# Kernel tuning notes

Hardware: AMD Instinct MI355X
Metric: run time of the kernel (lower is better)

Reference implementation:

```python
import math
import jax, jax.numpy as jnp
import numpy as np

H = 16  # num_heads

def get_alibi_slopes(n):
    def pow2_slopes(n):
        start = 2 ** (-2 ** (-(math.log2(n) - 3)))
        return [start * start ** i for i in range(n)]
    if math.log2(n).is_integer():
        return pow2_slopes(n)
    c = 2 ** math.floor(math.log2(n))
    return pow2_slopes(c) + get_alibi_slopes(2 * c)[0::2][: n - c]

def alibi_bias(num_heads, L, dtype=jnp.float32):
    slopes = jnp.asarray(get_alibi_slopes(num_heads), dtype=dtype)  # [H]
    pos = jnp.arange(L)
    rel = (pos[None, :] - pos[:, None]).astype(dtype)               # [L, L] = x - y
    bias = slopes[:, None, None] * rel[None, :, :]                  # [H, L, L]
    causal = pos[None, :] <= pos[:, None]                           # tril mask
    return jnp.where(causal[None, :, :], bias, -jnp.inf)


def setup_inputs() -> dict:
    key = jax.random.key(0)
    ks = jax.random.split(key, 4)
    D = 1024
    B, L = 2, 2048
    s_in = 1.0 / math.sqrt(D)
    return {
        "x": jax.random.normal(ks[0], (B, L, D), dtype=jnp.float32),
        "w_in": jax.random.normal(ks[1], (D, 3 * D), dtype=jnp.float32) * s_in,
        "b_in": jnp.zeros((3 * D,), dtype=jnp.float32),
        "w_out": jax.random.normal(ks[2], (D, D), dtype=jnp.float32) * s_in,
        "b_out": jnp.zeros((D,), dtype=jnp.float32),
    }


def reference(x, w_in, b_in, w_out, b_out):
    B, L, D = x.shape
    dh = D // H
    qkv = x @ w_in + b_in                                   # [B, L, 3D]
    q, k, v = jnp.split(qkv, 3, axis=-1)
    # [B, L, D] -> [B, H, L, dh]
    def heads(t):
        return t.reshape(B, L, H, dh).transpose(0, 2, 1, 3)
    q, k, v = heads(q), heads(k), heads(v)
    scores = jnp.einsum("bhqd,bhkd->bhqk", q, k) / math.sqrt(dh)
    scores = scores + alibi_bias(H, L, scores.dtype)[None]  # [B, H, L, L]
    attn = jax.nn.softmax(scores, axis=-1)
    out = jnp.einsum("bhqk,bhkd->bhqd", attn, v)            # [B, H, L, dh]
    out = out.transpose(0, 2, 1, 3).reshape(B, L, D)
    return out @ w_out + b_out
```

## Files before the change

### kernel.cpp

```cpp
#include <hip/hip_runtime.h>
#include <stdint.h>
#include <math.h>

#define NH 16
#define DH 64
#define SEQ 2048
#define DMODEL 1024

typedef short short8 __attribute__((ext_vector_type(8)));
typedef short short4v __attribute__((ext_vector_type(4)));
typedef float f32x4 __attribute__((ext_vector_type(4)));
typedef __bf16 bf16x4 __attribute__((ext_vector_type(4)));

__device__ __forceinline__ short f2bf(float f) {
  __bf16 h = (__bf16)f;
  return __builtin_bit_cast(short, h);
}
__device__ __forceinline__ short4v cvt4(f32x4 v) {
  bf16x4 b = __builtin_convertvector(v, bf16x4);
  return __builtin_bit_cast(short4v, b);
}
__device__ __forceinline__ float fast_exp2(float x) {
#if __has_builtin(__builtin_amdgcn_exp2f)
  return __builtin_amdgcn_exp2f(x);
#else
  return exp2f(x);
#endif
}

typedef const __attribute__((address_space(1))) uint32_t* gp_t;
typedef __attribute__((address_space(3))) uint32_t* lp_t;
__device__ __forceinline__ void async16(const short* g, short* l) {
  __builtin_amdgcn_global_load_lds((gp_t)g, (lp_t)l, 16, 0, 0);
}

__device__ __forceinline__ void transpose_tile(const float* __restrict__ in,
                                               short* __restrict__ out, int R, int C,
                                               int t, int tilesX, int tid) {
  __shared__ float tile[32][33];
  const int tx = tid & 31, ty = tid >> 5;
  const int c0 = (t % tilesX) * 32, r0 = (t / tilesX) * 32;
#pragma unroll
  for (int i = 0; i < 4; ++i)
    tile[ty + i * 8][tx] = in[(size_t)(r0 + ty + i * 8) * C + c0 + tx];
  __syncthreads();
#pragma unroll
  for (int i = 0; i < 4; ++i)
    out[(size_t)(c0 + ty + i * 8) * R + r0 + tx] = f2bf(tile[tx][ty + i * 8]);
}

__global__ void k_prep(const float* __restrict__ x, short* __restrict__ xb,
                       const float* __restrict__ w_in, short* __restrict__ w_in_t,
                       const float* __restrict__ w_out, short* __restrict__ w_out_t) {
  const int tid = threadIdx.x;
  const int blk = blockIdx.x;
  if (blk < 4096) {
    const int i = blk * 256 + tid;
    f32x4 v = ((const f32x4*)x)[i];
    ((short4v*)xb)[i] = cvt4(v);
  } else if (blk < 4096 + 3072) {
    transpose_tile(w_in, w_in_t, 1024, 3072, blk - 4096, 96, tid);
  } else {
    transpose_tile(w_out, w_out_t, 1024, 1024, blk - 7168, 32, tid);
  }
}

template <int MODE>
__launch_bounds__(256, 3)
__global__ void k_gemm(const short* __restrict__ A, const short* __restrict__ Bt,
                       const float* __restrict__ bias, float* __restrict__ Cf,
                       short* __restrict__ qo, short* __restrict__ ko,
                       short* __restrict__ vo) {
  constexpr int KD = 1024;
  __shared__ __align__(16) short As[128 * 64];
  __shared__ __align__(16) short Bs[128 * 64];
  const int tid = threadIdx.x;
  const int wave = tid >> 6, lane = tid & 63;
  const int quad = lane >> 4, l16 = lane & 15;
  const int wm = wave >> 1, wn = wave & 1;
  const int tM = blockIdx.y * 128, tN = blockIdx.x * 128;

  const short* pA[4];
  const short* pB[4];
  short* lA[4];
  short* lB[4];
#pragma unroll
  for (int t = 0; t < 4; ++t) {
    const int c = t * 256 + tid;
    const int row = c >> 3, gch = (c & 7) ^ (row & 7);
    pA[t] = A + (size_t)(tM + row) * KD + gch * 8;
    pB[t] = Bt + (size_t)(tN + row) * KD + gch * 8;
    lA[t] = &As[c * 8];
    lB[t] = &Bs[c * 8];
  }

  const int sw = l16 & 7;
  const int col0 = (quad ^ sw) << 3;
  const int col1 = col0 ^ 32;

  f32x4 acc[4][4] = {};

  for (int k0 = 0; k0 < KD; k0 += 64) {
    __syncthreads();
#pragma unroll
    for (int t = 0; t < 4; ++t) {
      async16(pA[t] + k0, lA[t]);
      async16(pB[t] + k0, lB[t]);
    }
    __syncthreads();
#pragma unroll
    for (int kh = 0; kh < 2; ++kh) {
      const int col = kh ? col1 : col0;
      short8 af[4], bfr[4];
#pragma unroll
      for (int i = 0; i < 4; ++i)
        af[i] = *(const short8*)&As[(wm * 64 + i * 16 + l16) * 64 + col];
#pragma unroll
      for (int i = 0; i < 4; ++i)
        bfr[i] = *(const short8*)&Bs[(wn * 64 + i * 16 + l16) * 64 + col];
#pragma unroll
      for (int i = 0; i < 4; ++i)
#pragma unroll
        for (int j = 0; j < 4; ++j)
          acc[i][j] = __builtin_amdgcn_mfma_f32_16x16x32_bf16(af[i], bfr[j], acc[i][j], 0, 0, 0);
    }
  }

  const int rbase = tM + wm * 64 + quad * 4;
#pragma unroll
  for (int i = 0; i < 4; ++i) {
#pragma unroll
    for (int j = 0; j < 4; ++j) {
      const int col = tN + wn * 64 + j * 16 + l16;
      const float bi = bias[col];
      if (MODE == 0) {
        const int which = col >> 10;
        const int h = (col & 1023) >> 6, d = col & 63;
        if (which == 2) {
          const int row0 = rbase + i * 16;
          const int b = row0 >> 11, li0 = row0 & 2047;
          f32x4 t;
#pragma unroll
          for (int rr = 0; rr < 4; ++rr) t[rr] = acc[i][j][rr] + bi;
          *(short4v*)&vo[(((size_t)(b * NH + h)) * DH + d) * SEQ + li0] = cvt4(t);
        } else {
          short* dst = (which == 0) ? qo : ko;
#pragma unroll
          for (int rr = 0; rr < 4; ++rr) {
            const int row = rbase + i * 16 + rr;
            const int b = row >> 11, li = row & 2047;
            dst[(((size_t)(b * NH + h)) * SEQ + li) * DH + d] = f2bf(acc[i][j][rr] + bi);
          }
        }
      } else {
#pragma unroll
        for (int rr = 0; rr < 4; ++rr) {
          const int row = rbase + i * 16 + rr;
          Cf[(size_t)row * DMODEL + col] = acc[i][j][rr] + bi;
        }
      }
    }
  }
}

__launch_bounds__(256)
__global__ void k_attn(const short* __restrict__ q, const short* __restrict__ k,
                       const short* __restrict__ vt, short* __restrict__ o) {
  __shared__ __align__(16) short Qs[64 * 64];
  __shared__ __align__(16) short Ks[64 * 64];
  __shared__ __align__(16) short Vs[64 * 64];
  __shared__ __align__(16) short Ps[4][16 * 64];
  const int tid = threadIdx.x;
  const int wave = tid >> 6, lane = tid & 63;
  const int quad = lane >> 4, l16 = lane & 15;
  const int sw = l16 & 7;
  const int qt = 31 - (blockIdx.x >> 5);
  const int bh = blockIdx.x & 31;
  const int h = bh & (NH - 1);
  const size_t base = (size_t)bh * SEQ * DH;
  const float LOG2E = 1.44269504088896f;
  const float slope2 = exp2f(-0.5f * (float)(h + 1)) * LOG2E;
  const float scale2 = 0.125f * LOG2E;
  const float FM = 12.0f;

  const int c0i = tid, c1i = 256 + tid;
  const int r0 = c0i >> 3, ch0 = (c0i & 7) ^ (r0 & 7);
  const int r1 = c1i >> 3, ch1 = (c1i & 7) ^ (r1 & 7);
  const int qk_off0 = r0 * DH + ch0 * 8;
  const int qk_off1 = r1 * DH + ch1 * 8;
  const int v_off0 = r0 * SEQ + ch0 * 8;
  const int v_off1 = r1 * SEQ + ch1 * 8;
  short* lQ0 = &Qs[c0i * 8]; short* lQ1 = &Qs[c1i * 8];
  short* lK0 = &Ks[c0i * 8]; short* lK1 = &Ks[c1i * 8];
  short* lV0 = &Vs[c0i * 8]; short* lV1 = &Vs[c1i * 8];

  const int col0 = ((quad ^ sw) << 3);
  const int col1 = col0 ^ 32;
  int psoff[4];
#pragma unroll
  for (int in = 0; in < 4; ++in)
    psoff[in] = l16 * 64 + (((2 * in + (quad >> 1)) ^ sw) << 3) + (quad & 1) * 4;
  const int qlim4 = wave * 16 + l16 - 4 * quad;
  const float s64 = slope2 * 64.0f;
  float rc[4];
#pragma unroll
  for (int r = 0; r < 4; ++r) rc[r] = slope2 * (float)r;

  const int q0 = qt * 64;
  {
    const short* qb = q + base + (size_t)q0 * DH;
    async16(qb + qk_off0, lQ0);
    async16(qb + qk_off1, lQ1);
  }
  __syncthreads();
  const short8 qb0 = *(const short8*)&Qs[(wave * 16 + l16) * 64 + col0];
  const short8 qb1 = *(const short8*)&Qs[(wave * 16 + l16) * 64 + col1];

  f32x4 accO[4] = {};
  float lsum = 0.f;
  const int qrow = q0 + wave * 16 + l16;
  const float qoff = -slope2 * (float)qrow - FM + slope2 * (float)(4 * quad);
  float inoff[4];
#pragma unroll
  for (int in = 0; in < 4; ++in)
    inoff[in] = qoff + slope2 * (float)(16 * in);

  const short* kp = k + base;
  const short* vp = vt + base;
  for (int kt = 0; kt <= qt; ++kt) {
    __syncthreads();
    async16(kp + qk_off0, lK0);
    async16(kp + qk_off1, lK1);
    async16(vp + v_off0, lV0);
    async16(vp + v_off1, lV1);
    kp += 64 * DH;
    vp += 64;
    __syncthreads();

    f32x4 s[4];
#pragma unroll
    for (int in = 0; in < 4; ++in) {
      const short8 ka0 = *(const short8*)&Ks[(in * 16 + l16) * 64 + col0];
      const short8 ka1 = *(const short8*)&Ks[(in * 16 + l16) * 64 + col1];
      f32x4 t = {};
      t = __builtin_amdgcn_mfma_f32_16x16x32_bf16(ka0, qb0, t, 0, 0, 0);
      t = __builtin_amdgcn_mfma_f32_16x16x32_bf16(ka1, qb1, t, 0, 0, 0);
      s[in] = t;
    }

    if (kt == qt) {
#pragma unroll
      for (int in = 0; in < 4; ++in) {
        f32x4 p;
#pragma unroll
        for (int r = 0; r < 4; ++r) {
          float val = fast_exp2(fmaf(s[in][r], scale2, inoff[in] + rc[r]));
          val = (16 * in + r <= qlim4) ? val : 0.f;
          p[r] = val;
          lsum += val;
        }
        *(short4v*)&Ps[wave][psoff[in]] = cvt4(p);
      }
    } else {
#pragma unroll
      for (int in = 0; in < 4; ++in) {
        f32x4 p;
#pragma unroll
        for (int r = 0; r < 4; ++r) {
          float val = fast_exp2(fmaf(s[in][r], scale2, inoff[in] + rc[r]));
          p[r] = val;
          lsum += val;
        }
        *(short4v*)&Ps[wave][psoff[in]] = cvt4(p);
      }
    }
#pragma unroll
    for (int in = 0; in < 4; ++in) inoff[in] += s64;

    const short8 pa0 = *(const short8*)&Ps[wave][l16 * 64 + col0];
    const short8 pa1 = *(const short8*)&Ps[wave][l16 * 64 + col1];
#pragma unroll
    for (int i = 0; i < 4; ++i) {
      const short8 va0 = *(const short8*)&Vs[(i * 16 + l16) * 64 + col0];
      const short8 va1 = *(const short8*)&Vs[(i * 16 + l16) * 64 + col1];
      accO[i] = __builtin_amdgcn_mfma_f32_16x16x32_bf16(va0, pa0, accO[i], 0, 0, 0);
      accO[i] = __builtin_amdgcn_mfma_f32_16x16x32_bf16(va1, pa1, accO[i], 0, 0, 0);
    }
  }

  lsum += __shfl_xor(lsum, 16, 64);
  lsum += __shfl_xor(lsum, 32, 64);
  const float inv = 1.0f / lsum;

  const int b = bh >> 4;
  short* ob = o + ((((size_t)b * SEQ + qrow) * NH + h) * DH + 4 * quad);
#pragma unroll
  for (int i = 0; i < 4; ++i) {
    f32x4 t;
#pragma unroll
    for (int r = 0; r < 4; ++r) t[r] = accO[i][r] * inv;
    *(short4v*)&ob[16 * i] = cvt4(t);
  }
}

extern "C" void kernel_launch(void* const* d_in, const int* in_sizes, int n_in,
                              void* d_out, int out_size, void* d_ws, size_t ws_size,
                              hipStream_t stream) {
  const float* x = (const float*)d_in[0];
  const float* w_in = (const float*)d_in[1];
  const float* b_in = (const float*)d_in[2];
  const float* w_out = (const float*)d_in[3];
  const float* b_out = (const float*)d_in[4];
  float* out = (float*)d_out;

  char* ws = (char*)d_ws;
  short* xb = (short*)(ws);
  short* w_in_t = (short*)(ws + (8u << 20));
  short* w_out_t = (short*)(ws + (14u << 20));
  short* qv = (short*)(ws + (16u << 20));
  short* kv = (short*)(ws + (24u << 20));
  short* vv = (short*)(ws + (32u << 20));
  short* ao = (short*)(ws + (40u << 20));

  k_prep<<<8192, 256, 0, stream>>>(x, xb, w_in, w_in_t, w_out, w_out_t);
  k_gemm<0><<<dim3(24, 32), 256, 0, stream>>>(xb, w_in_t, b_in, nullptr, qv, kv, vv);
  k_attn<<<1024, 256, 0, stream>>>(qv, kv, vv, ao);
  k_gemm<1><<<dim3(8, 32), 256, 0, stream>>>(ao, w_out_t, b_out, out, nullptr, nullptr, nullptr);
}
```

Measured before the change: 173.8 us.

## Load K/V fragments directly to registers, prefetch K, compute row sums via MFMA

The attention kernel drops the shared-memory staging of Q, K and V tiles and the two block-wide barriers per iteration. Each wave now loads its MFMA operand fragments straight from global memory into registers, and K for the next tile is prefetched by double-buffering registers. The softmax denominator is computed with an extra MFMA against a vector of ones instead of per-lane sums plus shuffles. The cost is redundant global loads across the four waves, since each wave loads the full K/V tile that was previously shared, plus higher register pressure. The row sum is also now taken from the bf16-rounded probabilities.

```diff
diff --git a/kernel.cpp b/kernel.cpp
--- a/kernel.cpp
+++ b/kernel.cpp
@@ -166,9 +166,6 @@
 __launch_bounds__(256)
 __global__ void k_attn(const short* __restrict__ q, const short* __restrict__ k,
                        const short* __restrict__ vt, short* __restrict__ o) {
-  __shared__ __align__(16) short Qs[64 * 64];
-  __shared__ __align__(16) short Ks[64 * 64];
-  __shared__ __align__(16) short Vs[64 * 64];
   __shared__ __align__(16) short Ps[4][16 * 64];
   const int tid = threadIdx.x;
   const int wave = tid >> 6, lane = tid & 63;
@@ -183,70 +180,67 @@
   const float scale2 = 0.125f * LOG2E;
   const float FM = 12.0f;
 
-  const int c0i = tid, c1i = 256 + tid;
-  const int r0 = c0i >> 3, ch0 = (c0i & 7) ^ (r0 & 7);
-  const int r1 = c1i >> 3, ch1 = (c1i & 7) ^ (r1 & 7);
-  const int qk_off0 = r0 * DH + ch0 * 8;
-  const int qk_off1 = r1 * DH + ch1 * 8;
-  const int v_off0 = r0 * SEQ + ch0 * 8;
-  const int v_off1 = r1 * SEQ + ch1 * 8;
-  short* lQ0 = &Qs[c0i * 8]; short* lQ1 = &Qs[c1i * 8];
-  short* lK0 = &Ks[c0i * 8]; short* lK1 = &Ks[c1i * 8];
-  short* lV0 = &Vs[c0i * 8]; short* lV1 = &Vs[c1i * 8];
-
-  const int col0 = ((quad ^ sw) << 3);
+  const int col0 = (quad ^ sw) << 3;
   const int col1 = col0 ^ 32;
   int psoff[4];
 #pragma unroll
   for (int in = 0; in < 4; ++in)
     psoff[in] = l16 * 64 + (((2 * in + (quad >> 1)) ^ sw) << 3) + (quad & 1) * 4;
   const int qlim4 = wave * 16 + l16 - 4 * quad;
+
+  const int q0 = qt * 64;
+  const int qrow = q0 + wave * 16 + l16;
+  const short* qp = q + base + (size_t)qrow * DH + quad * 8;
+  const short8 qb0 = *(const short8*)qp;
+  const short8 qb1 = *(const short8*)(qp + 32);
+
+  short8 ones;
+#pragma unroll
+  for (int j = 0; j < 8; ++j) ones[j] = (short)0x3F80;
+
+  f32x4 accO[4] = {};
+  f32x4 accL = {};
+  const float qoff = -slope2 * (float)qrow - FM + slope2 * (float)(4 * quad);
+  float inoff[4];
+#pragma unroll
+  for (int in = 0; in < 4; ++in)
+    inoff[in] = qoff + slope2 * (float)(16 * in);
   const float s64 = slope2 * 64.0f;
   float rc[4];
 #pragma unroll
   for (int r = 0; r < 4; ++r) rc[r] = slope2 * (float)r;
 
-  const int q0 = qt * 64;
-  {
-    const short* qb = q + base + (size_t)q0 * DH;
-    async16(qb + qk_off0, lQ0);
-    async16(qb + qk_off1, lQ1);
-  }
-  __syncthreads();
-  const short8 qb0 = *(const short8*)&Qs[(wave * 16 + l16) * 64 + col0];
-  const short8 qb1 = *(const short8*)&Qs[(wave * 16 + l16) * 64 + col1];
-
-  f32x4 accO[4] = {};
-  float lsum = 0.f;
-  const int qrow = q0 + wave * 16 + l16;
-  const float qoff = -slope2 * (float)qrow - FM + slope2 * (float)(4 * quad);
-  float inoff[4];
-#pragma unroll
-  for (int in = 0; in < 4; ++in)
-    inoff[in] = qoff + slope2 * (float)(16 * in);
-
-  const short* kp = k + base;
-  const short* vp = vt + base;
-  for (int kt = 0; kt <= qt; ++kt) {
-    __syncthreads();
-    async16(kp + qk_off0, lK0);
-    async16(kp + qk_off1, lK1);
-    async16(vp + v_off0, lV0);
-    async16(vp + v_off1, lV1);
-    kp += 64 * DH;
-    vp += 64;
-    __syncthreads();
-
+  const short* kfb = k + base + (size_t)l16 * DH + quad * 8;
+  const short* vfb = vt + base + (size_t)l16 * SEQ + quad * 8;
+
+  auto loadK = [&](int kt, short8* kr) {
+    const short* p = kfb + (size_t)(kt * 64) * DH;
+#pragma unroll
+    for (int in = 0; in < 4; ++in) {
+      kr[2 * in] = *(const short8*)(p + (size_t)(in * 16) * DH);
+      kr[2 * in + 1] = *(const short8*)(p + (size_t)(in * 16) * DH + 32);
+    }
+  };
+
+  auto step = [&](int kt, const short8* kr, short8* kn, bool pf) {
     f32x4 s[4];
 #pragma unroll
     for (int in = 0; in < 4; ++in) {
-      const short8 ka0 = *(const short8*)&Ks[(in * 16 + l16) * 64 + col0];
-      const short8 ka1 = *(const short8*)&Ks[(in * 16 + l16) * 64 + col1];
       f32x4 t = {};
-      t = __builtin_amdgcn_mfma_f32_16x16x32_bf16(ka0, qb0, t, 0, 0, 0);
-      t = __builtin_amdgcn_mfma_f32_16x16x32_bf16(ka1, qb1, t, 0, 0, 0);
+      t = __builtin_amdgcn_mfma_f32_16x16x32_bf16(kr[2 * in], qb0, t, 0, 0, 0);
+      t = __builtin_amdgcn_mfma_f32_16x16x32_bf16(kr[2 * in + 1], qb1, t, 0, 0, 0);
       s[in] = t;
     }
+    short8 vr[8];
+    {
+      const short* p = vfb + kt * 64;
+#pragma unroll
+      for (int i = 0; i < 4; ++i) {
+        vr[2 * i] = *(const short8*)(p + (size_t)(i * 16) * SEQ);
+        vr[2 * i + 1] = *(const short8*)(p + (size_t)(i * 16) * SEQ + 32);
+      }
+    }
+    if (pf) loadK(kt + 1, kn);
 
     if (kt == qt) {
 #pragma unroll
@@ -255,9 +249,7 @@
 #pragma unroll
         for (int r = 0; r < 4; ++r) {
           float val = fast_exp2(fmaf(s[in][r], scale2, inoff[in] + rc[r]));
-          val = (16 * in + r <= qlim4) ? val : 0.f;
-          p[r] = val;
-          lsum += val;
+          p[r] = (16 * in + r <= qlim4) ? val : 0.f;
         }
         *(short4v*)&Ps[wave][psoff[in]] = cvt4(p);
       }
@@ -266,11 +258,8 @@
       for (int in = 0; in < 4; ++in) {
         f32x4 p;
 #pragma unroll
-        for (int r = 0; r < 4; ++r) {
-          float val = fast_exp2(fmaf(s[in][r], scale2, inoff[in] + rc[r]));
-          p[r] = val;
-          lsum += val;
-        }
+        for (int r = 0; r < 4; ++r)
+          p[r] = fast_exp2(fmaf(s[in][r], scale2, inoff[in] + rc[r]));
         *(short4v*)&Ps[wave][psoff[in]] = cvt4(p);
       }
     }
@@ -279,19 +268,26 @@
 
     const short8 pa0 = *(const short8*)&Ps[wave][l16 * 64 + col0];
     const short8 pa1 = *(const short8*)&Ps[wave][l16 * 64 + col1];
+    accL = __builtin_amdgcn_mfma_f32_16x16x32_bf16(ones, pa0, accL, 0, 0, 0);
+    accL = __builtin_amdgcn_mfma_f32_16x16x32_bf16(ones, pa1, accL, 0, 0, 0);
 #pragma unroll
     for (int i = 0; i < 4; ++i) {
-      const short8 va0 = *(const short8*)&Vs[(i * 16 + l16) * 64 + col0];
-      const short8 va1 = *(const short8*)&Vs[(i * 16 + l16) * 64 + col1];
-      accO[i] = __builtin_amdgcn_mfma_f32_16x16x32_bf16(va0, pa0, accO[i], 0, 0, 0);
-      accO[i] = __builtin_amdgcn_mfma_f32_16x16x32_bf16(va1, pa1, accO[i], 0, 0, 0);
-    }
-  }
-
-  lsum += __shfl_xor(lsum, 16, 64);
-  lsum += __shfl_xor(lsum, 32, 64);
-  const float inv = 1.0f / lsum;
-
+      accO[i] = __builtin_amdgcn_mfma_f32_16x16x32_bf16(vr[2 * i], pa0, accO[i], 0, 0, 0);
+      accO[i] = __builtin_amdgcn_mfma_f32_16x16x32_bf16(vr[2 * i + 1], pa1, accO[i], 0, 0, 0);
+    }
+  };
+
+  short8 kA[8], kB[8];
+  loadK(0, kA);
+  int kt = 0;
+  for (;;) {
+    step(kt, kA, kB, kt < qt);
+    if (++kt > qt) break;
+    step(kt, kB, kA, kt < qt);
+    if (++kt > qt) break;
+  }
+
+  const float inv = 1.0f / accL[0];
   const int b = bh >> 4;
   short* ob = o + ((((size_t)b * SEQ + qrow) * NH + h) * DH + 4 * quad);
 #pragma unroll
```

After: 250.2 us. 43.9% more time.

## Double-buffer K/V tiles in attention, load Q from global, MFMA row sums

Applied to the files above, without the earlier changes.

Double-buffers the K and V shared-memory tiles so the async load of the next key block overlaps compute on the current one, using one barrier per iteration instead of two. Q fragments are loaded straight from global memory into registers, dropping the Q shared tile and its barrier. The softmax denominator now comes from an MFMA against a vector of bf16 ones instead of per-lane scalar adds and cross-lane shuffles. This doubles K/V LDS use and sums bf16-rounded probabilities, which matches what the PV product sees but changes rounding.

```diff
diff --git a/kernel.cpp b/kernel.cpp
--- a/kernel.cpp
+++ b/kernel.cpp
@@ -166,9 +166,8 @@
 __launch_bounds__(256)
 __global__ void k_attn(const short* __restrict__ q, const short* __restrict__ k,
                        const short* __restrict__ vt, short* __restrict__ o) {
-  __shared__ __align__(16) short Qs[64 * 64];
-  __shared__ __align__(16) short Ks[64 * 64];
-  __shared__ __align__(16) short Vs[64 * 64];
+  __shared__ __align__(16) short Ks[2][64 * 64];
+  __shared__ __align__(16) short Vs[2][64 * 64];
   __shared__ __align__(16) short Ps[4][16 * 64];
   const int tid = threadIdx.x;
   const int wave = tid >> 6, lane = tid & 63;
@@ -190,9 +189,6 @@
   const int qk_off1 = r1 * DH + ch1 * 8;
   const int v_off0 = r0 * SEQ + ch0 * 8;
   const int v_off1 = r1 * SEQ + ch1 * 8;
-  short* lQ0 = &Qs[c0i * 8]; short* lQ1 = &Qs[c1i * 8];
-  short* lK0 = &Ks[c0i * 8]; short* lK1 = &Ks[c1i * 8];
-  short* lV0 = &Vs[c0i * 8]; short* lV1 = &Vs[c1i * 8];
 
   const int col0 = ((quad ^ sw) << 3);
   const int col1 = col0 ^ 32;
@@ -201,47 +197,56 @@
   for (int in = 0; in < 4; ++in)
     psoff[in] = l16 * 64 + (((2 * in + (quad >> 1)) ^ sw) << 3) + (quad & 1) * 4;
   const int qlim4 = wave * 16 + l16 - 4 * quad;
+
+  const int q0 = qt * 64;
+  const int qrow = q0 + wave * 16 + l16;
+  const short* qp = q + base + (size_t)qrow * DH + quad * 8;
+  const short8 qb0 = *(const short8*)qp;
+  const short8 qb1 = *(const short8*)(qp + 32);
+
+  short8 ones;
+#pragma unroll
+  for (int j = 0; j < 8; ++j) ones[j] = (short)0x3F80;
+
+  f32x4 accO[4] = {};
+  f32x4 accL = {};
+  const float qoff = -slope2 * (float)qrow - FM + slope2 * (float)(4 * quad);
+  float inoff[4];
+#pragma unroll
+  for (int in = 0; in < 4; ++in)
+    inoff[in] = qoff + slope2 * (float)(16 * in);
   const float s64 = slope2 * 64.0f;
   float rc[4];
 #pragma unroll
   for (int r = 0; r < 4; ++r) rc[r] = slope2 * (float)r;
 
-  const int q0 = qt * 64;
-  {
-    const short* qb = q + base + (size_t)q0 * DH;
-    async16(qb + qk_off0, lQ0);
-    async16(qb + qk_off1, lQ1);
-  }
-  __syncthreads();
-  const short8 qb0 = *(const short8*)&Qs[(wave * 16 + l16) * 64 + col0];
-  const short8 qb1 = *(const short8*)&Qs[(wave * 16 + l16) * 64 + col1];
-
-  f32x4 accO[4] = {};
-  float lsum = 0.f;
-  const int qrow = q0 + wave * 16 + l16;
-  const float qoff = -slope2 * (float)qrow - FM + slope2 * (float)(4 * quad);
-  float inoff[4];
-#pragma unroll
-  for (int in = 0; in < 4; ++in)
-    inoff[in] = qoff + slope2 * (float)(16 * in);
-
   const short* kp = k + base;
   const short* vp = vt + base;
+
+  async16(kp + qk_off0, &Ks[0][c0i * 8]);
+  async16(kp + qk_off1, &Ks[0][c1i * 8]);
+  async16(vp + v_off0, &Vs[0][c0i * 8]);
+  async16(vp + v_off1, &Vs[0][c1i * 8]);
+  kp += 64 * DH;
+  vp += 64;
+  __syncthreads();
+
   for (int kt = 0; kt <= qt; ++kt) {
-    __syncthreads();
-    async16(kp + qk_off0, lK0);
-    async16(kp + qk_off1, lK1);
-    async16(vp + v_off0, lV0);
-    async16(vp + v_off1, lV1);
-    kp += 64 * DH;
-    vp += 64;
-    __syncthreads();
+    const int cur = kt & 1, nxt = cur ^ 1;
+    if (kt < qt) {
+      async16(kp + qk_off0, &Ks[nxt][c0i * 8]);
+      async16(kp + qk_off1, &Ks[nxt][c1i * 8]);
+      async16(vp + v_off0, &Vs[nxt][c0i * 8]);
+      async16(vp + v_off1, &Vs[nxt][c1i * 8]);
+      kp += 64 * DH;
+      vp += 64;
+    }
 
     f32x4 s[4];
 #pragma unroll
     for (int in = 0; in < 4; ++in) {
-      const short8 ka0 = *(const short8*)&Ks[(in * 16 + l16) * 64 + col0];
-      const short8 ka1 = *(const short8*)&Ks[(in * 16 + l16) * 64 + col1];
+      const short8 ka0 = *(const short8*)&Ks[cur][(in * 16 + l16) * 64 + col0];
+      const short8 ka1 = *(const short8*)&Ks[cur][(in * 16 + l16) * 64 + col1];
       f32x4 t = {};
       t = __builtin_amdgcn_mfma_f32_16x16x32_bf16(ka0, qb0, t, 0, 0, 0);
       t = __builtin_amdgcn_mfma_f32_16x16x32_bf16(ka1, qb1, t, 0, 0, 0);
@@ -255,9 +260,7 @@
 #pragma unroll
         for (int r = 0; r < 4; ++r) {
           float val = fast_exp2(fmaf(s[in][r], scale2, inoff[in] + rc[r]));
-          val = (16 * in + r <= qlim4) ? val : 0.f;
-          p[r] = val;
-          lsum += val;
+          p[r] = (16 * in + r <= qlim4) ? val : 0.f;
         }
         *(short4v*)&Ps[wave][psoff[in]] = cvt4(p);
       }
@@ -266,11 +269,8 @@
       for (int in = 0; in < 4; ++in) {
         f32x4 p;
 #pragma unroll
-        for (int r = 0; r < 4; ++r) {
-          float val = fast_exp2(fmaf(s[in][r], scale2, inoff[in] + rc[r]));
-          p[r] = val;
-          lsum += val;
-        }
+        for (int r = 0; r < 4; ++r)
+          p[r] = fast_exp2(fmaf(s[in][r], scale2, inoff[in] + rc[r]));
         *(short4v*)&Ps[wave][psoff[in]] = cvt4(p);
       }
     }
@@ -279,19 +279,19 @@
 
     const short8 pa0 = *(const short8*)&Ps[wave][l16 * 64 + col0];
     const short8 pa1 = *(const short8*)&Ps[wave][l16 * 64 + col1];
+    accL = __builtin_amdgcn_mfma_f32_16x16x32_bf16(ones, pa0, accL, 0, 0, 0);
+    accL = __builtin_amdgcn_mfma_f32_16x16x32_bf16(ones, pa1, accL, 0, 0, 0);
 #pragma unroll
     for (int i = 0; i < 4; ++i) {
-      const short8 va0 = *(const short8*)&Vs[(i * 16 + l16) * 64 + col0];
-      const short8 va1 = *(const short8*)&Vs[(i * 16 + l16) * 64 + col1];
+      const short8 va0 = *(const short8*)&Vs[cur][(i * 16 + l16) * 64 + col0];
+      const short8 va1 = *(const short8*)&Vs[cur][(i * 16 + l16) * 64 + col1];
       accO[i] = __builtin_amdgcn_mfma_f32_16x16x32_bf16(va0, pa0, accO[i], 0, 0, 0);
       accO[i] = __builtin_amdgcn_mfma_f32_16x16x32_bf16(va1, pa1, accO[i], 0, 0, 0);
     }
-  }
-
-  lsum += __shfl_xor(lsum, 16, 64);
-  lsum += __shfl_xor(lsum, 32, 64);
-  const float inv = 1.0f / lsum;
-
+    __syncthreads();
+  }
+
+  const float inv = 1.0f / accL[0];
   const int b = bh >> 4;
   short* ob = o + ((((size_t)b * SEQ + qrow) * NH + h) * DH + 4 * quad);
 #pragma unroll
```

New measurement: 169.1 us. 1.03x faster.
